# Performance work log

Hardware: AMD Instinct MI355X
Metric: run time of the kernel (lower is better)

The kernel has to match this reference:

```python
import jax, jax.numpy as jnp
import numpy as np


def setup_inputs() -> dict:
    key = jax.random.key(0)
    k1, k2, k3 = jax.random.split(key, 3)
    B, L, D = 4, 4096, 1024
    inputs = jax.random.normal(k1, (B, L, D), dtype=jnp.float32)
    # nn.Linear(2D, 2D): weight [out=2D, in=2D], bias [2D]
    W_gate = jax.random.normal(k2, (2 * D, 2 * D), dtype=jnp.float32) * (1.0 / np.sqrt(2 * D))
    b_gate = jax.random.normal(k3, (2 * D,), dtype=jnp.float32) * 0.01
    return {"inputs": inputs, "W_gate": W_gate, "b_gate": b_gate}


def reference(inputs, W_gate, b_gate):
    B, L, D = inputs.shape
    # Cumulative average: tril(ones)/arange mask matmul == prefix-mean (linear time)
    denom = jnp.arange(1, L + 1, dtype=inputs.dtype)[None, :, None]  # [1, L, 1]
    average_outputs = jnp.cumsum(inputs, axis=1) / denom  # [B, L, D]
    # Gating linear on concat(inputs, avg): y = x @ W^T + b
    cat = jnp.concatenate([inputs, average_outputs], axis=-1)  # [B, L, 2D]
    gating = jnp.einsum('bld,ed->ble', cat, W_gate) + b_gate  # [B, L, 2D]
    input_gate, forget_gate = jnp.split(gating, 2, axis=-1)
    gating_outputs = (jax.nn.sigmoid(input_gate) * inputs
                      + jax.nn.sigmoid(forget_gate) * average_outputs)
    return gating_outputs, average_outputs
```

## Files before the change

### kernel.cpp

```cpp
#include <hip/hip_runtime.h>

#define B_   4
#define L_   4096
#define D_   1024
#define ROWS (B_ * L_)
#define K2   (2 * D_)
#define BLD  (ROWS * D_)
#define CH   64
#define NC   64

typedef __attribute__((ext_vector_type(8))) short s8v;
typedef __attribute__((ext_vector_type(4))) float f4v;

__device__ __forceinline__ unsigned short f2bf(float f) {
    unsigned int u = __float_as_uint(f);
    u += 0x7FFFu + ((u >> 16) & 1u);
    return (unsigned short)(u >> 16);
}

__device__ __forceinline__ float sigmoidf_(float v) {
    return 1.0f / (1.0f + __expf(-v));
}

__device__ __forceinline__ void llds16(const void* g, void* l) {
    __builtin_amdgcn_global_load_lds(
        (const __attribute__((address_space(1))) unsigned int*)(g),
        (__attribute__((address_space(3))) unsigned int*)(l),
        16, 0, 0);
}


__global__ void partial_sums(const float4* __restrict__ x4, float4* __restrict__ part4) {
    int bid = blockIdx.x;
    int c = bid & 63, b = bid >> 6;
    int t = threadIdx.x;
    const float4* p = x4 + ((size_t)(b * L_ + c * CH) * 256 + t);
    float4 s; s.x = 0.f; s.y = 0.f; s.z = 0.f; s.w = 0.f;
#pragma unroll 8
    for (int i = 0; i < CH; ++i) {
        float4 v = p[(size_t)i * 256];
        s.x += v.x; s.y += v.y; s.z += v.z; s.w += v.w;
    }
    part4[(size_t)bid * 256 + t] = s;
}

__global__ void apply_scan(const float4* __restrict__ x4, const float4* __restrict__ part4,
                           float4* __restrict__ avg4, ushort4* __restrict__ A4) {
    __shared__ float inv[CH];
    int bid = blockIdx.x;
    int c = bid & 63, b = bid >> 6;
    int t = threadIdx.x;
    if (t < CH) inv[t] = 1.0f / (float)(c * CH + t + 1);

    float4 s; s.x = 0.f; s.y = 0.f; s.z = 0.f; s.w = 0.f;
    for (int cc = 0; cc < c; ++cc) {
        float4 v = part4[((size_t)(b * NC + cc)) * 256 + t];
        s.x += v.x; s.y += v.y; s.z += v.z; s.w += v.w;
    }
    __syncthreads();

    size_t row0 = (size_t)b * L_ + (size_t)c * CH;
    const float4* px = x4 + (row0 * 256 + t);
    float4*       pa = avg4 + (row0 * 256 + t);
    ushort4*      pA = A4 + (row0 * 512 + t);
#pragma unroll 4
    for (int i = 0; i < CH; ++i) {
        float4 v = px[(size_t)i * 256];
        s.x += v.x; s.y += v.y; s.z += v.z; s.w += v.w;
        float r = inv[i];
        float4 av; av.x = s.x * r; av.y = s.y * r; av.z = s.z * r; av.w = s.w * r;
        pa[(size_t)i * 256] = av;
        ushort4 ux; ux.x = f2bf(v.x);  ux.y = f2bf(v.y);  ux.z = f2bf(v.z);  ux.w = f2bf(v.w);
        ushort4 ua; ua.x = f2bf(av.x); ua.y = f2bf(av.y); ua.z = f2bf(av.z); ua.w = f2bf(av.w);
        pA[(size_t)i * 512]       = ux;
        pA[(size_t)i * 512 + 256] = ua;
    }
}

__global__ void conv_w(const float4* __restrict__ W, ushort4* __restrict__ Wbf) {
    int t = blockIdx.x * 256 + threadIdx.x;
    float4 v = W[t];
    ushort4 o;
    o.x = f2bf(v.x); o.y = f2bf(v.y); o.z = f2bf(v.z); o.w = f2bf(v.w);
    Wbf[t] = o;
}

__global__ __launch_bounds__(256, 2) void gemm_gated(
        const unsigned short* __restrict__ Abf, const unsigned short* __restrict__ Wbf,
        const float* __restrict__ x, const float* __restrict__ avg,
        const float* __restrict__ bg, float* __restrict__ out) {
    __shared__ __attribute__((aligned(16))) unsigned short sA [128 * 32];
    __shared__ __attribute__((aligned(16))) unsigned short sB0[128 * 32];
    __shared__ __attribute__((aligned(16))) unsigned short sB1[128 * 32];

    const int t    = threadIdx.x;
    const int w    = t >> 6;
    const int lane = t & 63;
    const int bid  = blockIdx.x;
    const int tileN = bid & 7, tileM = bid >> 3;
    const int row0 = tileM * 128, col0 = tileN * 128;
    const int wm = w >> 1, wn = w & 1;
    const int quad = lane >> 4, lcol = lane & 15;

    f4v acc0[4][4], acc1[4][4];
#pragma unroll
    for (int i = 0; i < 4; ++i)
#pragma unroll
        for (int j = 0; j < 4; ++j)
#pragma unroll
            for (int r = 0; r < 4; ++r) { acc0[i][j][r] = 0.f; acc1[i][j][r] = 0.f; }

    const int c0 = t, c1 = 256 + t;
    const unsigned short* gA0 = Abf + ((size_t)(row0 + (c0 >> 2)) * K2 + (c0 & 3) * 8);
    const unsigned short* gA1 = Abf + ((size_t)(row0 + (c1 >> 2)) * K2 + (c1 & 3) * 8);
    const unsigned short* gB0a = Wbf + ((size_t)(col0 + (c0 >> 2)) * K2 + (c0 & 3) * 8);
    const unsigned short* gB0b = Wbf + ((size_t)(col0 + (c1 >> 2)) * K2 + (c1 & 3) * 8);
    const unsigned short* gB1a = Wbf + ((size_t)(col0 + 1024 + (c0 >> 2)) * K2 + (c0 & 3) * 8);
    const unsigned short* gB1b = Wbf + ((size_t)(col0 + 1024 + (c1 >> 2)) * K2 + (c1 & 3) * 8);
    unsigned short* lA0  = &sA [w * 512];
    unsigned short* lA1  = &sA [2048 + w * 512];
    unsigned short* lB0a = &sB0[w * 512];
    unsigned short* lB0b = &sB0[2048 + w * 512];
    unsigned short* lB1a = &sB1[w * 512];
    unsigned short* lB1b = &sB1[2048 + w * 512];

    for (int k0 = 0; k0 < K2; k0 += 32) {
        __syncthreads();
        llds16(gA0  + k0, lA0);
        llds16(gA1  + k0, lA1);
        llds16(gB0a + k0, lB0a);
        llds16(gB0b + k0, lB0b);
        llds16(gB1a + k0, lB1a);
        llds16(gB1b + k0, lB1b);
        __syncthreads();

        s8v af[4], bf0[4], bf1[4];
#pragma unroll
        for (int i = 0; i < 4; ++i)
            af[i] = *(const s8v*)&sA[(wm * 64 + i * 16 + lcol) * 32 + quad * 8];
#pragma unroll
        for (int j = 0; j < 4; ++j) {
            bf0[j] = *(const s8v*)&sB0[(wn * 64 + j * 16 + lcol) * 32 + quad * 8];
            bf1[j] = *(const s8v*)&sB1[(wn * 64 + j * 16 + lcol) * 32 + quad * 8];
        }
#pragma unroll
        for (int i = 0; i < 4; ++i)
#pragma unroll
            for (int j = 0; j < 4; ++j) {
                acc0[i][j] = __builtin_amdgcn_mfma_f32_16x16x32_bf16(af[i], bf0[j], acc0[i][j], 0, 0, 0);
                acc1[i][j] = __builtin_amdgcn_mfma_f32_16x16x32_bf16(af[i], bf1[j], acc1[i][j], 0, 0, 0);
            }
    }

    float b1v[4], b2v[4];
#pragma unroll
    for (int j = 0; j < 4; ++j) {
        int cc = col0 + wn * 64 + j * 16 + lcol;
        b1v[j] = bg[cc];
        b2v[j] = bg[1024 + cc];
    }
#pragma unroll
    for (int i = 0; i < 4; ++i) {
#pragma unroll
        for (int j = 0; j < 4; ++j) {
            int rr = row0 + wm * 64 + i * 16 + quad * 4;
            int cc = col0 + wn * 64 + j * 16 + lcol;
#pragma unroll
            for (int r = 0; r < 4; ++r) {
                size_t off = (size_t)(rr + r) * D_ + cc;
                float gi = sigmoidf_(acc0[i][j][r] + b1v[j]);
                float gf = sigmoidf_(acc1[i][j][r] + b2v[j]);
                out[off] = gi * x[off] + gf * avg[off];
            }
        }
    }
}

extern "C" void kernel_launch(void* const* d_in, const int* in_sizes, int n_in,
                              void* d_out, int out_size, void* d_ws, size_t ws_size,
                              hipStream_t stream) {
    const float* x  = (const float*)d_in[0];
    const float* W  = (const float*)d_in[1];
    const float* bg = (const float*)d_in[2];
    float* out = (float*)d_out;
    float* avg = out + (size_t)BLD;

    char* ws = (char*)d_ws;
    unsigned short* Abf = (unsigned short*)(ws);
    unsigned short* Wbf = (unsigned short*)(ws + (size_t)67108864);
    float4* prt4 = (float4*)(ws + (size_t)67108864);

    partial_sums<<<dim3(256), dim3(256), 0, stream>>>((const float4*)x, prt4);
    apply_scan<<<dim3(256), dim3(256), 0, stream>>>((const float4*)x, prt4,
                                                    (float4*)avg, (ushort4*)Abf);
    conv_w<<<dim3(4096), dim3(256), 0, stream>>>((const float4*)W, (ushort4*)Wbf);
    gemm_gated<<<dim3(1024), dim3(256), 0, stream>>>(Abf, Wbf, x, avg, bg, out);
}
```

Before: 379.8 us.

## Pipeline GEMM with 4-stage LDS ring, 512-thread 256x128 tiles, fuse weight conversion

The gated GEMM now uses 512-thread blocks covering 256x128 output tiles. A 4-deep LDS ring buffer stages A and B through async global-to-LDS loads issued ahead of the MFMA work, with explicit vmcnt waits, raw barriers and setprio around the MFMA bursts. The LDS layout is XOR-swizzled to avoid bank conflicts, and blocks are remapped so neighbouring blocks share tiles for better L2 reuse. The weight bf16 conversion is merged into the partial-sum kernel to save a launch. The cost is a larger LDS footprint (128KB per block) and fragile hand-written synchronisation.

```diff
diff --git a/kernel.cpp b/kernel.cpp
--- a/kernel.cpp
+++ b/kernel.cpp
@@ -17,31 +17,39 @@
     u += 0x7FFFu + ((u >> 16) & 1u);
     return (unsigned short)(u >> 16);
 }
-
 __device__ __forceinline__ float sigmoidf_(float v) {
     return 1.0f / (1.0f + __expf(-v));
 }
-
 __device__ __forceinline__ void llds16(const void* g, void* l) {
     __builtin_amdgcn_global_load_lds(
         (const __attribute__((address_space(1))) unsigned int*)(g),
         (__attribute__((address_space(3))) unsigned int*)(l),
         16, 0, 0);
 }
-
-
-__global__ void partial_sums(const float4* __restrict__ x4, float4* __restrict__ part4) {
+#define MEMFENCE asm volatile("" ::: "memory")
+#define SBAR do { MEMFENCE; __builtin_amdgcn_s_barrier(); MEMFENCE; } while (0)
+
+
+__global__ void prep1(const float4* __restrict__ x4, float4* __restrict__ part4,
+                      const float4* __restrict__ W, ushort4* __restrict__ Wbf) {
     int bid = blockIdx.x;
-    int c = bid & 63, b = bid >> 6;
     int t = threadIdx.x;
-    const float4* p = x4 + ((size_t)(b * L_ + c * CH) * 256 + t);
-    float4 s; s.x = 0.f; s.y = 0.f; s.z = 0.f; s.w = 0.f;
+    if (bid < 256) {
+        int c = bid & 63, b = bid >> 6;
+        const float4* p = x4 + ((size_t)(b * L_ + c * CH) * 256 + t);
+        float4 s; s.x = 0.f; s.y = 0.f; s.z = 0.f; s.w = 0.f;
 #pragma unroll 8
-    for (int i = 0; i < CH; ++i) {
-        float4 v = p[(size_t)i * 256];
-        s.x += v.x; s.y += v.y; s.z += v.z; s.w += v.w;
-    }
-    part4[(size_t)bid * 256 + t] = s;
+        for (int i = 0; i < CH; ++i) {
+            float4 v = p[(size_t)i * 256];
+            s.x += v.x; s.y += v.y; s.z += v.z; s.w += v.w;
+        }
+        part4[(size_t)bid * 256 + t] = s;
+    } else {
+        int i = (bid - 256) * 256 + t;
+        float4 v = W[i];
+        ushort4 o; o.x = f2bf(v.x); o.y = f2bf(v.y); o.z = f2bf(v.z); o.w = f2bf(v.w);
+        Wbf[i] = o;
+    }
 }
 
 __global__ void apply_scan(const float4* __restrict__ x4, const float4* __restrict__ part4,
@@ -77,31 +85,23 @@
     }
 }
 
-__global__ void conv_w(const float4* __restrict__ W, ushort4* __restrict__ Wbf) {
-    int t = blockIdx.x * 256 + threadIdx.x;
-    float4 v = W[t];
-    ushort4 o;
-    o.x = f2bf(v.x); o.y = f2bf(v.y); o.z = f2bf(v.z); o.w = f2bf(v.w);
-    Wbf[t] = o;
-}
-
-__global__ __launch_bounds__(256, 2) void gemm_gated(
+__global__ __launch_bounds__(512, 2) void gemm_gated8(
         const unsigned short* __restrict__ Abf, const unsigned short* __restrict__ Wbf,
         const float* __restrict__ x, const float* __restrict__ avg,
         const float* __restrict__ bg, float* __restrict__ out) {
-    __shared__ __attribute__((aligned(16))) unsigned short sA [128 * 32];
-    __shared__ __attribute__((aligned(16))) unsigned short sB0[128 * 32];
-    __shared__ __attribute__((aligned(16))) unsigned short sB1[128 * 32];
+    __shared__ __attribute__((aligned(16))) unsigned short S[4 * 2 * 8192];
 
     const int t    = threadIdx.x;
     const int w    = t >> 6;
     const int lane = t & 63;
-    const int bid  = blockIdx.x;
-    const int tileN = bid & 7, tileM = bid >> 3;
-    const int row0 = tileM * 128, col0 = tileN * 128;
     const int wm = w >> 1, wn = w & 1;
     const int quad = lane >> 4, lcol = lane & 15;
 
+    const int bid = blockIdx.x;
+    const int swz = (bid & 7) * 64 + (bid >> 3);
+    const int tileN = swz & 7, tileM = swz >> 3;
+    const int row0 = tileM * 256, col0 = tileN * 128;
+
     f4v acc0[4][4], acc1[4][4];
 #pragma unroll
     for (int i = 0; i < 4; ++i)
@@ -110,46 +110,83 @@
 #pragma unroll
             for (int r = 0; r < 4; ++r) { acc0[i][j][r] = 0.f; acc1[i][j][r] = 0.f; }
 
-    const int c0 = t, c1 = 256 + t;
-    const unsigned short* gA0 = Abf + ((size_t)(row0 + (c0 >> 2)) * K2 + (c0 & 3) * 8);
-    const unsigned short* gA1 = Abf + ((size_t)(row0 + (c1 >> 2)) * K2 + (c1 & 3) * 8);
-    const unsigned short* gB0a = Wbf + ((size_t)(col0 + (c0 >> 2)) * K2 + (c0 & 3) * 8);
-    const unsigned short* gB0b = Wbf + ((size_t)(col0 + (c1 >> 2)) * K2 + (c1 & 3) * 8);
-    const unsigned short* gB1a = Wbf + ((size_t)(col0 + 1024 + (c0 >> 2)) * K2 + (c0 & 3) * 8);
-    const unsigned short* gB1b = Wbf + ((size_t)(col0 + 1024 + (c1 >> 2)) * K2 + (c1 & 3) * 8);
-    unsigned short* lA0  = &sA [w * 512];
-    unsigned short* lA1  = &sA [2048 + w * 512];
-    unsigned short* lB0a = &sB0[w * 512];
-    unsigned short* lB0b = &sB0[2048 + w * 512];
-    unsigned short* lB1a = &sB1[w * 512];
-    unsigned short* lB1b = &sB1[2048 + w * 512];
-
-    for (int k0 = 0; k0 < K2; k0 += 32) {
-        __syncthreads();
-        llds16(gA0  + k0, lA0);
-        llds16(gA1  + k0, lA1);
-        llds16(gB0a + k0, lB0a);
-        llds16(gB0b + k0, lB0b);
-        llds16(gB1a + k0, lB1a);
-        llds16(gB1b + k0, lB1b);
-        __syncthreads();
-
-        s8v af[4], bf0[4], bf1[4];
+    const int qA0 = t, qA1 = 512 + t;
+    const int p0 = qA0 ^ ((qA0 >> 2) & 3);
+    const int p1 = qA1 ^ ((qA1 >> 2) & 3);
+    const int m0 = p0 >> 2, k0e = (p0 & 3) * 8;
+    const int m1 = p1 >> 2, k1e = (p1 & 3) * 8;
+    const unsigned short* gA0 = Abf + (size_t)(row0 + m0) * K2 + k0e;
+    const unsigned short* gA1 = Abf + (size_t)(row0 + m1) * K2 + k1e;
+    const unsigned short* gB0 = Wbf + (size_t)(col0 + (m0 & 127) + (m0 >> 7) * 1024) * K2 + k0e;
+    const unsigned short* gB1 = Wbf + (size_t)(col0 + (m1 & 127) + (m1 >> 7) * 1024) * K2 + k1e;
+
+    int aoff[4], boff[2][4];
+#pragma unroll
+    for (int i = 0; i < 4; ++i)
+        aoff[i] = ((((wm * 64 + i * 16 + lcol) * 64) + quad * 16) ^ ((lcol & 3) << 4)) >> 1;
+#pragma unroll
+    for (int h = 0; h < 2; ++h)
+#pragma unroll
+        for (int j = 0; j < 4; ++j)
+            boff[h][j] = ((((h * 128 + wn * 64 + j * 16 + lcol) * 64) + quad * 16) ^ ((lcol & 3) << 4)) >> 1;
+
+#pragma unroll
+    for (int tt = 0; tt < 3; ++tt) {
+        unsigned short* dA = S + tt * 16384;
+        unsigned short* dB = S + tt * 16384 + 8192;
+        llds16(gA0 + tt * 32, dA + qA0 * 8);
+        llds16(gA1 + tt * 32, dA + qA1 * 8);
+        llds16(gB0 + tt * 32, dB + qA0 * 8);
+        llds16(gB1 + tt * 32, dB + qA1 * 8);
+    }
+    asm volatile("s_waitcnt vmcnt(8)" ::: "memory");
+    SBAR;
+
+#pragma unroll 4
+    for (int tau = 0; tau < 64; ++tau) {
+        const unsigned short* bA = S + (tau & 3) * 16384;
+        const unsigned short* bB = bA + 8192;
+        const int st = tau + 3;
+        unsigned short* dA = S + (st & 3) * 16384;
+        unsigned short* dB = dA + 8192;
+        const bool do_stage = st < 64;
+        const int ko = st * 32;
+
+        s8v af[4], bf[4];
+#pragma unroll
+        for (int i = 0; i < 4; ++i) af[i] = *(const s8v*)(bA + aoff[i]);
+#pragma unroll
+        for (int j = 0; j < 4; ++j) bf[j] = *(const s8v*)(bB + boff[0][j]);
+        if (do_stage) {
+            llds16(gA0 + ko, dA + qA0 * 8);
+            llds16(gA1 + ko, dA + qA1 * 8);
+        }
+        SBAR;
+        __builtin_amdgcn_s_setprio(1);
 #pragma unroll
         for (int i = 0; i < 4; ++i)
-            af[i] = *(const s8v*)&sA[(wm * 64 + i * 16 + lcol) * 32 + quad * 8];
-#pragma unroll
-        for (int j = 0; j < 4; ++j) {
-            bf0[j] = *(const s8v*)&sB0[(wn * 64 + j * 16 + lcol) * 32 + quad * 8];
-            bf1[j] = *(const s8v*)&sB1[(wn * 64 + j * 16 + lcol) * 32 + quad * 8];
-        }
+#pragma unroll
+            for (int j = 0; j < 4; ++j)
+                acc0[i][j] = __builtin_amdgcn_mfma_f32_16x16x32_bf16(af[i], bf[j], acc0[i][j], 0, 0, 0);
+        __builtin_amdgcn_s_setprio(0);
+        SBAR;
+
+#pragma unroll
+        for (int j = 0; j < 4; ++j) bf[j] = *(const s8v*)(bB + boff[1][j]);
+        if (do_stage) {
+            llds16(gB0 + ko, dB + qA0 * 8);
+            llds16(gB1 + ko, dB + qA1 * 8);
+        }
+        asm volatile("s_waitcnt vmcnt(8)" ::: "memory");
+        SBAR;
+        __builtin_amdgcn_s_setprio(1);
 #pragma unroll
         for (int i = 0; i < 4; ++i)
 #pragma unroll
-            for (int j = 0; j < 4; ++j) {
-                acc0[i][j] = __builtin_amdgcn_mfma_f32_16x16x32_bf16(af[i], bf0[j], acc0[i][j], 0, 0, 0);
-                acc1[i][j] = __builtin_amdgcn_mfma_f32_16x16x32_bf16(af[i], bf1[j], acc1[i][j], 0, 0, 0);
-            }
+            for (int j = 0; j < 4; ++j)
+                acc1[i][j] = __builtin_amdgcn_mfma_f32_16x16x32_bf16(af[i], bf[j], acc1[i][j], 0, 0, 0);
+        __builtin_amdgcn_s_setprio(0);
+        SBAR;
     }
 
     float b1v[4], b2v[4];
@@ -188,11 +225,11 @@
     char* ws = (char*)d_ws;
     unsigned short* Abf = (unsigned short*)(ws);
     unsigned short* Wbf = (unsigned short*)(ws + (size_t)67108864);
-    float4* prt4 = (float4*)(ws + (size_t)67108864);
-
-    partial_sums<<<dim3(256), dim3(256), 0, stream>>>((const float4*)x, prt4);
-    apply_scan<<<dim3(256), dim3(256), 0, stream>>>((const float4*)x, prt4,
+    float4*         prt = (float4*)(ws + (size_t)75497472);
+
+    prep1<<<dim3(4352), dim3(256), 0, stream>>>((const float4*)x, prt,
+                                                (const float4*)W, (ushort4*)Wbf);
+    apply_scan<<<dim3(256), dim3(256), 0, stream>>>((const float4*)x, prt,
                                                     (float4*)avg, (ushort4*)Abf);
-    conv_w<<<dim3(4096), dim3(256), 0, stream>>>((const float4*)W, (ushort4*)Wbf);
-    gemm_gated<<<dim3(1024), dim3(256), 0, stream>>>(Abf, Wbf, x, avg, bg, out);
-}
+    gemm_gated8<<<dim3(512), dim3(512), 0, stream>>>(Abf, Wbf, x, avg, bg, out);
+}
```

Measured after the change: 365.7 us. -3.7%, faster.
